# Optimization experiments

Measured on AMD Instinct MI355X. Metric: run time of the kernel, lower is better.

Reference implementation:

```python
import jax, jax.numpy as jnp
import numpy as np

N = 10000
E = 640000
IN_CH = 512
OUT_CH = 256
K = 2


def setup_inputs() -> dict:
    key = jax.random.key(0)
    k1, k2, k3, k4, k5 = jax.random.split(key, 5)
    x = jax.random.normal(k1, (N, IN_CH), dtype=jnp.float32)
    edge_index = jax.random.randint(k2, (2, E), 0, N, dtype=jnp.int64)
    lin_w = jax.random.normal(k3, (OUT_CH, IN_CH), dtype=jnp.float32) * (1.0 / np.sqrt(IN_CH))
    lin_b = jax.random.normal(k4, (OUT_CH,), dtype=jnp.float32) * 0.01
    weights = jax.random.uniform(k5, (K,), dtype=jnp.float32)
    return {"x": x, "edge_index": edge_index, "lin_w": lin_w, "lin_b": lin_b, "weights": weights}


def reference(x, edge_index, lin_w, lin_b, weights):
    n = x.shape[0]
    row, col = edge_index[0], edge_index[1]
    # deg = bincount(row); symmetric-normalized edge weights
    deg = jax.ops.segment_sum(jnp.ones(row.shape[0], dtype=x.dtype), row, num_segments=n)
    deg_inv_sqrt = jnp.where(deg > 0, jax.lax.rsqrt(deg), 0.0)
    norm = deg_inv_sqrt[row] * deg_inv_sqrt[col]  # [E]

    def spmm(h):
        # y[i] = sum_{e: row[e]==i} norm[e] * h[col[e]]
        return jax.ops.segment_sum(norm[:, None] * h[col], row, num_segments=n)

    out = x @ lin_w.T + lin_b  # [N, OUT_CH]
    # Faithful ARMA loop: x_k starts from the CURRENT accumulated `out` each hop-group
    for k in range(K):
        x_k = out
        for _ in range(k + 1):
            x_k = spmm(x_k)
        out = out + weights[k] * x_k
    return out
```

## Files before the change

### kernel.cpp

```cpp
#include <hip/hip_runtime.h>

#define N_NODES 10000
#define E_EDGES 640000
#define IN_CH   512
#define OUT_CH  256
#define HALF_CH 128
#define CSR_CAP (E_EDGES + 16 * N_NODES + 128)
#define G_GEMM_X 157
#define G_GEMM  (G_GEMM_X * 2)
#define HBLK    125
#define EPB     5120

typedef short bf16x8 __attribute__((ext_vector_type(8)));
typedef float f32x4  __attribute__((ext_vector_type(4)));

__device__ __forceinline__ unsigned short f2b(float f) {
    unsigned int u = __float_as_uint(f);
    return (unsigned short)((u + 0x7FFFu + ((u >> 16) & 1u)) >> 16);
}
__device__ __forceinline__ float lo16(unsigned int u) { return __uint_as_float(u << 16); }
__device__ __forceinline__ float hi16(unsigned int u) { return __uint_as_float(u & 0xFFFF0000u); }
__device__ __forceinline__ float b2f(unsigned short u) { return __uint_as_float(((unsigned int)u) << 16); }

__global__ __launch_bounds__(256) void hist_rank(const int* __restrict__ row,
                                                 int* __restrict__ cnt,
                                                 unsigned short* __restrict__ rank) {
    __shared__ int hist[N_NODES];
    int b = blockIdx.x, tid = threadIdx.x;
    for (int i = tid; i < N_NODES; i += 256) hist[i] = 0;
    __syncthreads();
    int ebase = b * EPB;
    #pragma unroll 4
    for (int i = tid; i < EPB; i += 256) {
        int r = row[ebase + i];
        rank[ebase + i] = (unsigned short)atomicAdd(&hist[r], 1);
    }
    __syncthreads();
    int* cb = cnt + (size_t)b * N_NODES;
    for (int i = tid; i < N_NODES; i += 256) cb[i] = hist[i];
}

__global__ __launch_bounds__(256) void alloc_a(int* __restrict__ cnt,
                                               int2* __restrict__ pd,
                                               float* __restrict__ dinv, float* __restrict__ sq,
                                               int* __restrict__ pads, int n) {
    int r = blockIdx.x * 4 + (threadIdx.x >> 6);
    int lane = threadIdx.x & 63;
    if (r >= n) return;
    int v0 = cnt[(size_t)lane * N_NODES + r];
    int v1 = (lane < HBLK - 64) ? cnt[(size_t)(64 + lane) * N_NODES + r] : 0;
    int s0 = v0, s1 = v1;
    #pragma unroll
    for (int off = 1; off < 64; off <<= 1) {
        int t0 = __shfl_up(s0, off, 64);
        int t1 = __shfl_up(s1, off, 64);
        if (lane >= off) { s0 += t0; s1 += t1; }
    }
    int tot0 = __shfl(s0, 63, 64);
    int d = tot0 + __shfl(s1, 63, 64);
    int pad = (d + 15) & ~15;
    cnt[(size_t)lane * N_NODES + r] = s0 - v0;
    if (lane < HBLK - 64) cnt[(size_t)(64 + lane) * N_NODES + r] = tot0 + s1 - v1;
    if (lane == 0) {
        dinv[r] = (d > 0) ? rsqrtf((float)d) : 0.0f;
        sq[r]   = (d > 0) ? sqrtf((float)d) : 0.0f;
        pd[r] = make_int2(d, pad);
        pads[r] = pad;
    }
}

__global__ __launch_bounds__(1024) void scan_pads(const int* __restrict__ pads,
                                                  int* __restrict__ rowstart, int n) {
    __shared__ int ls[1024];
    int t = threadIdx.x;
    int base = t * 10;
    int loc[10];
    int sum = 0;
    if (base < n) {
        #pragma unroll
        for (int i = 0; i < 10; i++) { loc[i] = pads[base + i]; sum += loc[i]; }
    }
    ls[t] = sum;
    __syncthreads();
    for (int off = 1; off < 1024; off <<= 1) {
        int v = (t >= off) ? ls[t - off] : 0;
        __syncthreads();
        ls[t] += v;
        __syncthreads();
    }
    if (base < n) {
        int run = ls[t] - sum;
        #pragma unroll
        for (int i = 0; i < 10; i++) { rowstart[base + i] = run; run += loc[i]; }
    }
}

__global__ __launch_bounds__(256) void alloc_b(const int* __restrict__ rowstart,
                                               const int2* __restrict__ pd,
                                               int2* __restrict__ seg,
                                               int* __restrict__ csr_col, int n) {
    int r = blockIdx.x * 4 + (threadIdx.x >> 6);
    int lane = threadIdx.x & 63;
    if (r >= n) return;
    int s = rowstart[r];
    int2 pd_ = pd[r];
    if (lane == 0) seg[r] = make_int2(s, s + pd_.y);
    int j = pd_.x + lane;
    if (j < pd_.y) csr_col[s + j] = N_NODES;
}

__global__ __launch_bounds__(256) void gemm_scatter(const float* __restrict__ x,
                                                    const float* __restrict__ w,
                                                    const float* __restrict__ bias,
                                                    const float* __restrict__ dinv,
                                                    unsigned short* __restrict__ h0b,
                                                    const int* __restrict__ row,
                                                    const int* __restrict__ col,
                                                    const int* __restrict__ base,
                                                    const int* __restrict__ rowstart,
                                                    const unsigned short* __restrict__ rank,
                                                    int* __restrict__ csr_col) {
    __shared__ __align__(16) char smem[40960];
    int bid = blockIdx.x;
    int tid = threadIdx.x;
    if (bid >= G_GEMM) {
        int sb = bid - G_GEMM;
        int* bs = (int*)smem;
        const int4* cb4 = (const int4*)(base + (size_t)sb * N_NODES);
        const int4* rs4 = (const int4*)rowstart;
        for (int i = tid; i < N_NODES / 4; i += 256) {
            int4 c = cb4[i];
            int4 r = rs4[i];
            int4 o;
            o.x = c.x + r.x; o.y = c.y + r.y; o.z = c.z + r.z; o.w = c.w + r.w;
            ((int4*)bs)[i] = o;
        }
        __syncthreads();
        int ebase = sb * EPB;
        #pragma unroll 4
        for (int i = tid; i < EPB; i += 256) {
            int e = ebase + i;
            int p = bs[row[e]] + (int)rank[e];
            csr_col[p] = col[e];
        }
        return;
    }
    typedef unsigned short us72[72];
    us72* As = (us72*)smem;
    us72* Bs = (us72*)(smem + 64 * 72 * 2);
    int bx = bid % G_GEMM_X;
    int plane = bid / G_GEMM_X;
    int wave = tid >> 6, lane = tid & 63, quad = lane >> 4, l16 = lane & 15;
    int row0 = bx * 64;
    int n0 = plane * 128;
    unsigned short* h0b_p = h0b + (size_t)plane * (N_NODES + 1) * HALF_CH;

    int ar = tid >> 2;
    int aseg = (tid & 3) * 16;
    int br = tid >> 1;
    int bseg = (tid & 1) * 32;

    f32x4 acc[8] = {};
    for (int k0 = 0; k0 < IN_CH; k0 += 64) {
        {
            int gr = row0 + ar;
            if (gr < N_NODES) {
                const float4* src = (const float4*)(x + (size_t)gr * IN_CH + k0 + aseg);
                #pragma unroll
                for (int i = 0; i < 4; i++) {
                    float4 v = src[i];
                    ushort4 o;
                    o.x = f2b(v.x); o.y = f2b(v.y); o.z = f2b(v.z); o.w = f2b(v.w);
                    *(ushort4*)&As[ar][aseg + i * 4] = o;
                }
            } else {
                ushort4 z = {0, 0, 0, 0};
                #pragma unroll
                for (int i = 0; i < 4; i++) *(ushort4*)&As[ar][aseg + i * 4] = z;
            }
        }
        {
            const float4* src = (const float4*)(w + (size_t)(n0 + br) * IN_CH + k0 + bseg);
            #pragma unroll
            for (int i = 0; i < 8; i++) {
                float4 v = src[i];
                ushort4 o;
                o.x = f2b(v.x); o.y = f2b(v.y); o.z = f2b(v.z); o.w = f2b(v.w);
                *(ushort4*)&Bs[br][bseg + i * 4] = o;
            }
        }
        __syncthreads();
        #pragma unroll
        for (int kk = 0; kk < 2; kk++) {
            bf16x8 a = *(const bf16x8*)&As[wave * 16 + l16][kk * 32 + quad * 8];
            #pragma unroll
            for (int t = 0; t < 8; t++) {
                bf16x8 b = *(const bf16x8*)&Bs[t * 16 + l16][kk * 32 + quad * 8];
                acc[t] = __builtin_amdgcn_mfma_f32_16x16x32_bf16(a, b, acc[t], 0, 0, 0);
            }
        }
        __syncthreads();
    }
    #pragma unroll
    for (int t = 0; t < 8; t++) {
        int lcol = t * 16 + l16;
        int col_ = n0 + lcol;
        float bv = bias[col_];
        #pragma unroll
        for (int r = 0; r < 4; r++) {
            int grow = row0 + wave * 16 + quad * 4 + r;
            if (grow < N_NODES) {
                float v = acc[t][r] + bv;
                h0b_p[(size_t)grow * HALF_CH + lcol] = f2b(v * dinv[grow]);
            }
        }
    }
    if (bx == 0 && tid < 64)
        ((unsigned int*)(h0b_p + (size_t)N_NODES * HALF_CH))[tid] = 0u;
}

__global__ __launch_bounds__(256) void spmm_kernel(const unsigned short* __restrict__ hb,
                                                   const int2* __restrict__ seg,
                                                   const int* __restrict__ csr_col,
                                                   const float* __restrict__ dinv,
                                                   const float* __restrict__ sq,
                                                   const unsigned short* __restrict__ prev_b,
                                                   const float* __restrict__ wts, int widx,
                                                   unsigned short* __restrict__ yb_out,
                                                   float* __restrict__ axpy_out,
                                                   unsigned short* __restrict__ axpyb_out,
                                                   int n) {
    int plane = blockIdx.x & 1;
    int node = (blockIdx.x >> 1) * 4 + (threadIdx.x >> 6);
    int lane = threadIdx.x & 63;
    if (node >= n) return;
    int sub = lane >> 4, l16 = lane & 15;
    size_t pstride = (size_t)(n + 1) * HALF_CH;
    const unsigned short* hp = hb + (size_t)plane * pstride;

    int2 se = seg[node];
    int s = se.x, e = se.y;
    float acc[8] = {0.f, 0.f, 0.f, 0.f, 0.f, 0.f, 0.f, 0.f};
    if (s < e) {
        int cA0 = csr_col[s + 0  + sub];
        int cA1 = csr_col[s + 4  + sub];
        int cA2 = csr_col[s + 8  + sub];
        int cA3 = csr_col[s + 12 + sub];
        uint4 vA0 = *(const uint4*)(hp + (size_t)cA0 * HALF_CH + l16 * 8);
        uint4 vA1 = *(const uint4*)(hp + (size_t)cA1 * HALF_CH + l16 * 8);
        uint4 vA2 = *(const uint4*)(hp + (size_t)cA2 * HALF_CH + l16 * 8);
        uint4 vA3 = *(const uint4*)(hp + (size_t)cA3 * HALF_CH + l16 * 8);
        int cB0 = csr_col[s + 16 + sub];
        int cB1 = csr_col[s + 20 + sub];
        int cB2 = csr_col[s + 24 + sub];
        int cB3 = csr_col[s + 28 + sub];
        int p = s;
        while (p + 16 < e) {
            uint4 vB0 = *(const uint4*)(hp + (size_t)cB0 * HALF_CH + l16 * 8);
            uint4 vB1 = *(const uint4*)(hp + (size_t)cB1 * HALF_CH + l16 * 8);
            uint4 vB2 = *(const uint4*)(hp + (size_t)cB2 * HALF_CH + l16 * 8);
            uint4 vB3 = *(const uint4*)(hp + (size_t)cB3 * HALF_CH + l16 * 8);
            int pn = p + 32;
            int cC0 = csr_col[pn + 0  + sub];
            int cC1 = csr_col[pn + 4  + sub];
            int cC2 = csr_col[pn + 8  + sub];
            int cC3 = csr_col[pn + 12 + sub];
            acc[0] += lo16(vA0.x) + lo16(vA1.x) + lo16(vA2.x) + lo16(vA3.x);
            acc[1] += hi16(vA0.x) + hi16(vA1.x) + hi16(vA2.x) + hi16(vA3.x);
            acc[2] += lo16(vA0.y) + lo16(vA1.y) + lo16(vA2.y) + lo16(vA3.y);
            acc[3] += hi16(vA0.y) + hi16(vA1.y) + hi16(vA2.y) + hi16(vA3.y);
            acc[4] += lo16(vA0.z) + lo16(vA1.z) + lo16(vA2.z) + lo16(vA3.z);
            acc[5] += hi16(vA0.z) + hi16(vA1.z) + hi16(vA2.z) + hi16(vA3.z);
            acc[6] += lo16(vA0.w) + lo16(vA1.w) + lo16(vA2.w) + lo16(vA3.w);
            acc[7] += hi16(vA0.w) + hi16(vA1.w) + hi16(vA2.w) + hi16(vA3.w);
            vA0 = vB0; vA1 = vB1; vA2 = vB2; vA3 = vB3;
            cB0 = cC0; cB1 = cC1; cB2 = cC2; cB3 = cC3;
            p += 16;
        }
        acc[0] += lo16(vA0.x) + lo16(vA1.x) + lo16(vA2.x) + lo16(vA3.x);
        acc[1] += hi16(vA0.x) + hi16(vA1.x) + hi16(vA2.x) + hi16(vA3.x);
        acc[2] += lo16(vA0.y) + lo16(vA1.y) + lo16(vA2.y) + lo16(vA3.y);
        acc[3] += hi16(vA0.y) + hi16(vA1.y) + hi16(vA2.y) + hi16(vA3.y);
        acc[4] += lo16(vA0.z) + lo16(vA1.z) + lo16(vA2.z) + lo16(vA3.z);
        acc[5] += hi16(vA0.z) + hi16(vA1.z) + hi16(vA2.z) + hi16(vA3.z);
        acc[6] += lo16(vA0.w) + lo16(vA1.w) + lo16(vA2.w) + lo16(vA3.w);
        acc[7] += hi16(vA0.w) + hi16(vA1.w) + hi16(vA2.w) + hi16(vA3.w);
    }
    #pragma unroll
    for (int k = 0; k < 8; k++) {
        acc[k] += __shfl_xor(acc[k], 16, 64);
        acc[k] += __shfl_xor(acc[k], 32, 64);
    }
    if (sub != 0) return;

    float di = dinv[node];
    float y[8];
    #pragma unroll
    for (int k = 0; k < 8; k++) y[k] = di * acc[k];

    size_t pbase = (size_t)plane * pstride + (size_t)node * HALF_CH + l16 * 8;
    size_t padrow = (size_t)plane * pstride + (size_t)n * HALF_CH + l16 * 8;
    if (yb_out) {
        ushort4 o0, o1;
        o0.x = f2b(di * y[0]); o0.y = f2b(di * y[1]); o0.z = f2b(di * y[2]); o0.w = f2b(di * y[3]);
        o1.x = f2b(di * y[4]); o1.y = f2b(di * y[5]); o1.z = f2b(di * y[6]); o1.w = f2b(di * y[7]);
        *(ushort4*)(yb_out + pbase) = o0;
        *(ushort4*)(yb_out + pbase + 4) = o1;
        if (node == 0) {
            ushort4 z = {0, 0, 0, 0};
            *(ushort4*)(yb_out + padrow) = z;
            *(ushort4*)(yb_out + padrow + 4) = z;
        }
    }
    if (prev_b) {
        float wk = wts[widx];
        float sqn = sq[node];
        ushort4 p0 = *(const ushort4*)(prev_b + pbase);
        ushort4 p1 = *(const ushort4*)(prev_b + pbase + 4);
        float o[8];
        o[0] = b2f(p0.x) * sqn + wk * y[0];
        o[1] = b2f(p0.y) * sqn + wk * y[1];
        o[2] = b2f(p0.z) * sqn + wk * y[2];
        o[3] = b2f(p0.w) * sqn + wk * y[3];
        o[4] = b2f(p1.x) * sqn + wk * y[4];
        o[5] = b2f(p1.y) * sqn + wk * y[5];
        o[6] = b2f(p1.z) * sqn + wk * y[6];
        o[7] = b2f(p1.w) * sqn + wk * y[7];
        if (axpy_out) {
            size_t fbase = (size_t)node * OUT_CH + plane * HALF_CH + l16 * 8;
            float4 f0 = {o[0], o[1], o[2], o[3]};
            float4 f1 = {o[4], o[5], o[6], o[7]};
            *(float4*)(axpy_out + fbase) = f0;
            *(float4*)(axpy_out + fbase + 4) = f1;
        }
        if (axpyb_out) {
            ushort4 b0, b1;
            b0.x = f2b(di * o[0]); b0.y = f2b(di * o[1]); b0.z = f2b(di * o[2]); b0.w = f2b(di * o[3]);
            b1.x = f2b(di * o[4]); b1.y = f2b(di * o[5]); b1.z = f2b(di * o[6]); b1.w = f2b(di * o[7]);
            *(ushort4*)(axpyb_out + pbase) = b0;
            *(ushort4*)(axpyb_out + pbase + 4) = b1;
            if (node == 0) {
                ushort4 z = {0, 0, 0, 0};
                *(ushort4*)(axpyb_out + padrow) = z;
                *(ushort4*)(axpyb_out + padrow + 4) = z;
            }
        }
    }
}

extern "C" void kernel_launch(void* const* d_in, const int* in_sizes, int n_in,
                              void* d_out, int out_size, void* d_ws, size_t ws_size,
                              hipStream_t stream) {
    const float* x     = (const float*)d_in[0];
    const int*   ei    = (const int*)d_in[1];
    const float* lin_w = (const float*)d_in[2];
    const float* lin_b = (const float*)d_in[3];
    const float* wts   = (const float*)d_in[4];
    float* out = (float*)d_out;

    char* ws = (char*)d_ws;
    size_t off = 0;
    auto alloc = [&](size_t bytes) -> void* {
        void* p = ws + off;
        off += (bytes + 255) & ~(size_t)255;
        return p;
    };
    int*   cnt      = (int*)  alloc((size_t)HBLK * N_NODES * 4);
    unsigned short* rank = (unsigned short*)alloc((size_t)E_EDGES * 2);
    int2*  pd       = (int2*) alloc((size_t)N_NODES * 8);
    int*   pads     = (int*)  alloc((size_t)N_NODES * 4);
    int*   rowstart = (int*)  alloc((size_t)N_NODES * 4);
    int2*  seg      = (int2*) alloc((size_t)N_NODES * 8);
    float* dinv     = (float*)alloc(N_NODES * 4);
    float* sq       = (float*)alloc(N_NODES * 4);
    int*   csr_col  = (int*)  alloc((size_t)CSR_CAP * 4);
    unsigned short* h0b   = (unsigned short*)alloc((size_t)2 * (N_NODES + 1) * HALF_CH * 2);
    unsigned short* out1b = (unsigned short*)alloc((size_t)2 * (N_NODES + 1) * HALF_CH * 2);
    unsigned short* t2b   = (unsigned short*)alloc((size_t)2 * (N_NODES + 1) * HALF_CH * 2);

    const int* row = ei;
    const int* col = ei + E_EDGES;

    hist_rank<<<HBLK, 256, 0, stream>>>(row, cnt, rank);
    alloc_a<<<(N_NODES + 3) / 4, 256, 0, stream>>>(cnt, pd, dinv, sq, pads, N_NODES);
    scan_pads<<<1, 1024, 0, stream>>>(pads, rowstart, N_NODES);
    alloc_b<<<(N_NODES + 3) / 4, 256, 0, stream>>>(rowstart, pd, seg, csr_col, N_NODES);

    gemm_scatter<<<G_GEMM + HBLK, 256, 0, stream>>>(x, lin_w, lin_b, dinv, h0b,
                                                    row, col, cnt, rowstart, rank, csr_col);

    int sgrid = 2 * ((N_NODES + 3) / 4);
    spmm_kernel<<<sgrid, 256, 0, stream>>>(h0b, seg, csr_col, dinv, sq, h0b,
                                           wts, 0, nullptr, nullptr, out1b, N_NODES);
    spmm_kernel<<<sgrid, 256, 0, stream>>>(out1b, seg, csr_col, dinv, sq, nullptr,
                                           wts, 0, t2b, nullptr, nullptr, N_NODES);
    spmm_kernel<<<sgrid, 256, 0, stream>>>(t2b, seg, csr_col, dinv, sq, out1b,
                                           wts, 1, nullptr, out, nullptr, N_NODES);
}
```

Before: 203.9 us.

## Co-schedule GEMM with histogram pass and defer dinv scaling to scatter kernel

Moves the dense GEMM so it runs in the same launch as the per-block row histogram, instead of with the CSR scatter. The GEMM now writes fp32 output without the degree scaling. A new scatter_scale kernel then does the CSR column scatter and, in the same launch, applies the dinv scaling and bf16 conversion. The aim is to hide the histogram's latency behind the GEMM. The cost is an extra fp32 intermediate buffer of about 10 MB written and read back, plus 2500 extra blocks.

```diff
diff --git a/kernel.cpp b/kernel.cpp
--- a/kernel.cpp
+++ b/kernel.cpp
@@ -10,6 +10,7 @@
 #define G_GEMM  (G_GEMM_X * 2)
 #define HBLK    125
 #define EPB     5120
+#define G_SCALE 2500
 
 typedef short bf16x8 __attribute__((ext_vector_type(8)));
 typedef float f32x4  __attribute__((ext_vector_type(4)));
@@ -22,127 +23,29 @@
 __device__ __forceinline__ float hi16(unsigned int u) { return __uint_as_float(u & 0xFFFF0000u); }
 __device__ __forceinline__ float b2f(unsigned short u) { return __uint_as_float(((unsigned int)u) << 16); }
 
-__global__ __launch_bounds__(256) void hist_rank(const int* __restrict__ row,
+__global__ __launch_bounds__(256) void gemm_hist(const float* __restrict__ x,
+                                                 const float* __restrict__ w,
+                                                 const float* __restrict__ bias,
+                                                 float* __restrict__ h0f,
+                                                 const int* __restrict__ row,
                                                  int* __restrict__ cnt,
                                                  unsigned short* __restrict__ rank) {
-    __shared__ int hist[N_NODES];
-    int b = blockIdx.x, tid = threadIdx.x;
-    for (int i = tid; i < N_NODES; i += 256) hist[i] = 0;
-    __syncthreads();
-    int ebase = b * EPB;
-    #pragma unroll 4
-    for (int i = tid; i < EPB; i += 256) {
-        int r = row[ebase + i];
-        rank[ebase + i] = (unsigned short)atomicAdd(&hist[r], 1);
-    }
-    __syncthreads();
-    int* cb = cnt + (size_t)b * N_NODES;
-    for (int i = tid; i < N_NODES; i += 256) cb[i] = hist[i];
-}
-
-__global__ __launch_bounds__(256) void alloc_a(int* __restrict__ cnt,
-                                               int2* __restrict__ pd,
-                                               float* __restrict__ dinv, float* __restrict__ sq,
-                                               int* __restrict__ pads, int n) {
-    int r = blockIdx.x * 4 + (threadIdx.x >> 6);
-    int lane = threadIdx.x & 63;
-    if (r >= n) return;
-    int v0 = cnt[(size_t)lane * N_NODES + r];
-    int v1 = (lane < HBLK - 64) ? cnt[(size_t)(64 + lane) * N_NODES + r] : 0;
-    int s0 = v0, s1 = v1;
-    #pragma unroll
-    for (int off = 1; off < 64; off <<= 1) {
-        int t0 = __shfl_up(s0, off, 64);
-        int t1 = __shfl_up(s1, off, 64);
-        if (lane >= off) { s0 += t0; s1 += t1; }
-    }
-    int tot0 = __shfl(s0, 63, 64);
-    int d = tot0 + __shfl(s1, 63, 64);
-    int pad = (d + 15) & ~15;
-    cnt[(size_t)lane * N_NODES + r] = s0 - v0;
-    if (lane < HBLK - 64) cnt[(size_t)(64 + lane) * N_NODES + r] = tot0 + s1 - v1;
-    if (lane == 0) {
-        dinv[r] = (d > 0) ? rsqrtf((float)d) : 0.0f;
-        sq[r]   = (d > 0) ? sqrtf((float)d) : 0.0f;
-        pd[r] = make_int2(d, pad);
-        pads[r] = pad;
-    }
-}
-
-__global__ __launch_bounds__(1024) void scan_pads(const int* __restrict__ pads,
-                                                  int* __restrict__ rowstart, int n) {
-    __shared__ int ls[1024];
-    int t = threadIdx.x;
-    int base = t * 10;
-    int loc[10];
-    int sum = 0;
-    if (base < n) {
-        #pragma unroll
-        for (int i = 0; i < 10; i++) { loc[i] = pads[base + i]; sum += loc[i]; }
-    }
-    ls[t] = sum;
-    __syncthreads();
-    for (int off = 1; off < 1024; off <<= 1) {
-        int v = (t >= off) ? ls[t - off] : 0;
-        __syncthreads();
-        ls[t] += v;
-        __syncthreads();
-    }
-    if (base < n) {
-        int run = ls[t] - sum;
-        #pragma unroll
-        for (int i = 0; i < 10; i++) { rowstart[base + i] = run; run += loc[i]; }
-    }
-}
-
-__global__ __launch_bounds__(256) void alloc_b(const int* __restrict__ rowstart,
-                                               const int2* __restrict__ pd,
-                                               int2* __restrict__ seg,
-                                               int* __restrict__ csr_col, int n) {
-    int r = blockIdx.x * 4 + (threadIdx.x >> 6);
-    int lane = threadIdx.x & 63;
-    if (r >= n) return;
-    int s = rowstart[r];
-    int2 pd_ = pd[r];
-    if (lane == 0) seg[r] = make_int2(s, s + pd_.y);
-    int j = pd_.x + lane;
-    if (j < pd_.y) csr_col[s + j] = N_NODES;
-}
-
-__global__ __launch_bounds__(256) void gemm_scatter(const float* __restrict__ x,
-                                                    const float* __restrict__ w,
-                                                    const float* __restrict__ bias,
-                                                    const float* __restrict__ dinv,
-                                                    unsigned short* __restrict__ h0b,
-                                                    const int* __restrict__ row,
-                                                    const int* __restrict__ col,
-                                                    const int* __restrict__ base,
-                                                    const int* __restrict__ rowstart,
-                                                    const unsigned short* __restrict__ rank,
-                                                    int* __restrict__ csr_col) {
     __shared__ __align__(16) char smem[40960];
     int bid = blockIdx.x;
     int tid = threadIdx.x;
     if (bid >= G_GEMM) {
-        int sb = bid - G_GEMM;
-        int* bs = (int*)smem;
-        const int4* cb4 = (const int4*)(base + (size_t)sb * N_NODES);
-        const int4* rs4 = (const int4*)rowstart;
-        for (int i = tid; i < N_NODES / 4; i += 256) {
-            int4 c = cb4[i];
-            int4 r = rs4[i];
-            int4 o;
-            o.x = c.x + r.x; o.y = c.y + r.y; o.z = c.z + r.z; o.w = c.w + r.w;
-            ((int4*)bs)[i] = o;
-        }
-        __syncthreads();
-        int ebase = sb * EPB;
-        #pragma unroll 4
+        int* hist = (int*)smem;
+        int b = bid - G_GEMM;
+        for (int i = tid; i < N_NODES; i += 256) hist[i] = 0;
+        __syncthreads();
+        int ebase = b * EPB;
         for (int i = tid; i < EPB; i += 256) {
-            int e = ebase + i;
-            int p = bs[row[e]] + (int)rank[e];
-            csr_col[p] = col[e];
-        }
+            int r = row[ebase + i];
+            rank[ebase + i] = (unsigned short)atomicAdd(&hist[r], 1);
+        }
+        __syncthreads();
+        int* cb = cnt + (size_t)b * N_NODES;
+        for (int i = tid; i < N_NODES; i += 256) cb[i] = hist[i];
         return;
     }
     typedef unsigned short us72[72];
@@ -153,7 +56,7 @@
     int wave = tid >> 6, lane = tid & 63, quad = lane >> 4, l16 = lane & 15;
     int row0 = bx * 64;
     int n0 = plane * 128;
-    unsigned short* h0b_p = h0b + (size_t)plane * (N_NODES + 1) * HALF_CH;
+    float* h0f_p = h0f + (size_t)plane * N_NODES * HALF_CH;
 
     int ar = tid >> 2;
     int aseg = (tid & 3) * 16;
@@ -204,19 +107,133 @@
     #pragma unroll
     for (int t = 0; t < 8; t++) {
         int lcol = t * 16 + l16;
-        int col_ = n0 + lcol;
-        float bv = bias[col_];
+        float bv = bias[n0 + lcol];
         #pragma unroll
         for (int r = 0; r < 4; r++) {
             int grow = row0 + wave * 16 + quad * 4 + r;
-            if (grow < N_NODES) {
-                float v = acc[t][r] + bv;
-                h0b_p[(size_t)grow * HALF_CH + lcol] = f2b(v * dinv[grow]);
-            }
-        }
-    }
-    if (bx == 0 && tid < 64)
-        ((unsigned int*)(h0b_p + (size_t)N_NODES * HALF_CH))[tid] = 0u;
+            if (grow < N_NODES)
+                h0f_p[(size_t)grow * HALF_CH + lcol] = acc[t][r] + bv;
+        }
+    }
+}
+
+__global__ __launch_bounds__(256) void alloc_a(int* __restrict__ cnt,
+                                               int2* __restrict__ pd,
+                                               float* __restrict__ dinv, float* __restrict__ sq,
+                                               int* __restrict__ pads, int n) {
+    int r = blockIdx.x * 4 + (threadIdx.x >> 6);
+    int lane = threadIdx.x & 63;
+    if (r >= n) return;
+    int v0 = cnt[(size_t)lane * N_NODES + r];
+    int v1 = (lane < HBLK - 64) ? cnt[(size_t)(64 + lane) * N_NODES + r] : 0;
+    int s0 = v0, s1 = v1;
+    #pragma unroll
+    for (int off = 1; off < 64; off <<= 1) {
+        int t0 = __shfl_up(s0, off, 64);
+        int t1 = __shfl_up(s1, off, 64);
+        if (lane >= off) { s0 += t0; s1 += t1; }
+    }
+    int tot0 = __shfl(s0, 63, 64);
+    int d = tot0 + __shfl(s1, 63, 64);
+    int pad = (d + 15) & ~15;
+    cnt[(size_t)lane * N_NODES + r] = s0 - v0;
+    if (lane < HBLK - 64) cnt[(size_t)(64 + lane) * N_NODES + r] = tot0 + s1 - v1;
+    if (lane == 0) {
+        dinv[r] = (d > 0) ? rsqrtf((float)d) : 0.0f;
+        sq[r]   = (d > 0) ? sqrtf((float)d) : 0.0f;
+        pd[r] = make_int2(d, pad);
+        pads[r] = pad;
+    }
+}
+
+__global__ __launch_bounds__(1024) void scan_pads(const int* __restrict__ pads,
+                                                  int* __restrict__ rowstart, int n) {
+    __shared__ int ls[1024];
+    int t = threadIdx.x;
+    int base = t * 10;
+    int loc[10];
+    int sum = 0;
+    if (base < n) {
+        #pragma unroll
+        for (int i = 0; i < 10; i++) { loc[i] = pads[base + i]; sum += loc[i]; }
+    }
+    ls[t] = sum;
+    __syncthreads();
+    for (int off = 1; off < 1024; off <<= 1) {
+        int v = (t >= off) ? ls[t - off] : 0;
+        __syncthreads();
+        ls[t] += v;
+        __syncthreads();
+    }
+    if (base < n) {
+        int run = ls[t] - sum;
+        #pragma unroll
+        for (int i = 0; i < 10; i++) { rowstart[base + i] = run; run += loc[i]; }
+    }
+}
+
+__global__ __launch_bounds__(256) void alloc_b(const int* __restrict__ rowstart,
+                                               const int2* __restrict__ pd,
+                                               int2* __restrict__ seg,
+                                               int* __restrict__ csr_col, int n) {
+    int r = blockIdx.x * 4 + (threadIdx.x >> 6);
+    int lane = threadIdx.x & 63;
+    if (r >= n) return;
+    int s = rowstart[r];
+    int2 pd_ = pd[r];
+    if (lane == 0) seg[r] = make_int2(s, s + pd_.y);
+    int j = pd_.x + lane;
+    if (j < pd_.y) csr_col[s + j] = N_NODES;
+}
+
+__global__ __launch_bounds__(256) void scatter_scale(const int* __restrict__ row,
+                                                     const int* __restrict__ col,
+                                                     const int* __restrict__ base,
+                                                     const int* __restrict__ rowstart,
+                                                     const unsigned short* __restrict__ rank,
+                                                     int* __restrict__ csr_col,
+                                                     const float* __restrict__ h0f,
+                                                     const float* __restrict__ dinv,
+                                                     unsigned short* __restrict__ h0b) {
+    int bid = blockIdx.x;
+    int tid = threadIdx.x;
+    size_t pstride = (size_t)(N_NODES + 1) * HALF_CH;
+    if (bid < HBLK) {
+        __shared__ int bs[N_NODES];
+        const int4* cb4 = (const int4*)(base + (size_t)bid * N_NODES);
+        const int4* rs4 = (const int4*)rowstart;
+        for (int i = tid; i < N_NODES / 4; i += 256) {
+            int4 c = cb4[i];
+            int4 r = rs4[i];
+            int4 o;
+            o.x = c.x + r.x; o.y = c.y + r.y; o.z = c.z + r.z; o.w = c.w + r.w;
+            ((int4*)bs)[i] = o;
+        }
+        __syncthreads();
+        int ebase = bid * EPB;
+        for (int i = tid; i < EPB; i += 256) {
+            int e = ebase + i;
+            int p = bs[row[e]] + (int)rank[e];
+            csr_col[p] = col[e];
+        }
+        return;
+    }
+    int idx = bid - HBLK;
+    int node = idx * 4 + (tid >> 6);
+    int lane = tid & 63;
+    float di = dinv[node];
+    #pragma unroll
+    for (int plane = 0; plane < 2; plane++) {
+        const float2* src = (const float2*)(h0f + (size_t)plane * N_NODES * HALF_CH
+                                            + (size_t)node * HALF_CH);
+        float2 v = src[lane];
+        unsigned int o = (unsigned int)f2b(v.x * di) | ((unsigned int)f2b(v.y * di) << 16);
+        ((unsigned int*)(h0b + (size_t)plane * pstride + (size_t)node * HALF_CH))[lane] = o;
+    }
+    if (idx == 0 && tid < 128) {
+        int plane = tid >> 6;
+        ((unsigned int*)(h0b + (size_t)plane * pstride + (size_t)N_NODES * HALF_CH))[tid & 63] = 0u;
+    }
 }
 
 __global__ __launch_bounds__(256) void spmm_kernel(const unsigned short* __restrict__ hb,
@@ -374,6 +391,7 @@
     float* dinv     = (float*)alloc(N_NODES * 4);
     float* sq       = (float*)alloc(N_NODES * 4);
     int*   csr_col  = (int*)  alloc((size_t)CSR_CAP * 4);
+    float* h0f      = (float*)alloc((size_t)2 * N_NODES * HALF_CH * 4);
     unsigned short* h0b   = (unsigned short*)alloc((size_t)2 * (N_NODES + 1) * HALF_CH * 2);
     unsigned short* out1b = (unsigned short*)alloc((size_t)2 * (N_NODES + 1) * HALF_CH * 2);
     unsigned short* t2b   = (unsigned short*)alloc((size_t)2 * (N_NODES + 1) * HALF_CH * 2);
@@ -381,13 +399,14 @@
     const int* row = ei;
     const int* col = ei + E_EDGES;
 
-    hist_rank<<<HBLK, 256, 0, stream>>>(row, cnt, rank);
+    gemm_hist<<<G_GEMM + HBLK, 256, 0, stream>>>(x, lin_w, lin_b, h0f, row, cnt, rank);
+
     alloc_a<<<(N_NODES + 3) / 4, 256, 0, stream>>>(cnt, pd, dinv, sq, pads, N_NODES);
     scan_pads<<<1, 1024, 0, stream>>>(pads, rowstart, N_NODES);
     alloc_b<<<(N_NODES + 3) / 4, 256, 0, stream>>>(rowstart, pd, seg, csr_col, N_NODES);
 
-    gemm_scatter<<<G_GEMM + HBLK, 256, 0, stream>>>(x, lin_w, lin_b, dinv, h0b,
-                                                    row, col, cnt, rowstart, rank, csr_col);
+    scatter_scale<<<HBLK + G_SCALE, 256, 0, stream>>>(row, col, cnt, rowstart, rank,
+                                                      csr_col, h0f, dinv, h0b);
 
     int sgrid = 2 * ((N_NODES + 3) / 4);
     spmm_kernel<<<sgrid, 256, 0, stream>>>(h0b, seg, csr_col, dinv, sq, h0b,
```

Measured after the change: 206.4 us. About the same (+1.3%).
